# Kernel tuning notes

Hardware: AMD Instinct MI355X
Metric: run time of the kernel (lower is better)

Reference implementation:

```python
import jax, jax.numpy as jnp
import numpy as np

N_SRC = 100000
N_DST = 20000
N_EDGES = 640000
D_IN = 128
D_OUT = 128


def setup_inputs() -> dict:
    key = jax.random.key(0)
    ks = jax.random.split(key, 6)
    feat_src = jax.random.normal(ks[0], (N_SRC, D_IN), dtype=jnp.float32)
    feat_dst = jax.random.normal(ks[1], (N_DST, D_IN), dtype=jnp.float32)
    src_idx = jax.random.randint(ks[2], (N_EDGES,), 0, N_SRC, dtype=jnp.int64 if jax.config.jax_enable_x64 else jnp.int32)
    dst_idx = jax.random.randint(ks[3], (N_EDGES,), 0, N_DST, dtype=jnp.int64 if jax.config.jax_enable_x64 else jnp.int32)
    # xavier-uniform-ish init scale for [out, in] Linear weights
    lim = float(np.sqrt(6.0 / (D_IN + D_OUT)))
    W_self = jax.random.uniform(ks[4], (D_OUT, D_IN), jnp.float32, -lim, lim)
    W_neigh = jax.random.uniform(ks[5], (D_OUT, D_IN), jnp.float32, -lim, lim)
    b_self = jnp.zeros((D_OUT,), jnp.float32)
    b_neigh = jnp.zeros((D_OUT,), jnp.float32)
    return {
        "feat_src": feat_src, "feat_dst": feat_dst,
        "src_idx": src_idx, "dst_idx": dst_idx,
        "W_self": W_self, "b_self": b_self,
        "W_neigh": W_neigh, "b_neigh": b_neigh,
    }


def reference(feat_src, feat_dst, src_idx, dst_idx, W_self, b_self, W_neigh, b_neigh):
    n_dst = feat_dst.shape[0]
    # message passing: copy_src + mean reduce over incoming edges per dst node
    msgs = feat_src[src_idx]                                   # [E, D_in]
    summed = jax.ops.segment_sum(msgs, dst_idx, num_segments=n_dst)  # [N_dst, D_in]
    deg = jax.ops.segment_sum(jnp.ones((src_idx.shape[0],), feat_src.dtype),
                              dst_idx, num_segments=n_dst)     # [N_dst]
    h_neigh = summed / jnp.maximum(deg, 1.0)[:, None]          # mean (0 for isolated)
    # rst = fc_self(h_self) + fc_neigh(h_neigh); no activation
    rst = (feat_dst @ W_self.T + b_self) + (h_neigh @ W_neigh.T + b_neigh)
    return rst
```

## Files before the change

### kernel.cpp

```cpp
#include <hip/hip_runtime.h>

#define D 128
#define NDST 20000
#define NHB 64
#define CAP 96

typedef __attribute__((ext_vector_type(8))) short short8;
typedef __attribute__((ext_vector_type(4))) float f32x4;
typedef __attribute__((ext_vector_type(2))) float f32x2;

__device__ __forceinline__ unsigned f2bf(float f) {
  unsigned x = __float_as_uint(f);
  return (x + 0x7FFFu + ((x >> 16) & 1u)) >> 16;
}
__device__ __forceinline__ unsigned pack2(float a, float b) {
  return f2bf(a) | (f2bf(b) << 16);
}
__device__ __forceinline__ unsigned pack_fp8x4(float a, float b, float c, float d) {
  int v = 0;
  v = __builtin_amdgcn_cvt_pk_fp8_f32(a, b, v, false);
  v = __builtin_amdgcn_cvt_pk_fp8_f32(c, d, v, true);
  return (unsigned)v;
}

__global__ __launch_bounds__(512) void k1(
    const int* __restrict__ dst_idx,
    const float* __restrict__ feat_src,
    const float* __restrict__ feat_dst,
    const float* __restrict__ W_self,
    const float* __restrict__ b_self,
    const float* __restrict__ b_neigh,
    unsigned char* __restrict__ blockHist8,
    unsigned short* __restrict__ rank16,
    unsigned char* __restrict__ fsrc8,
    float* __restrict__ out,
    int n_src, int n_dst, int n_edges, int EPB, int NCB)
{
  __shared__ __align__(16) unsigned char ldsb[43520];
  const int tid = threadIdx.x;
  const int bid = blockIdx.x;

  if (bid < NHB) {
    unsigned int* hist = reinterpret_cast<unsigned int*>(ldsb);
    for (int i = tid; i < NDST / 16; i += 512)
      reinterpret_cast<uint4*>(hist)[i] = make_uint4(0u, 0u, 0u, 0u);
    __syncthreads();
    const int e0 = bid * EPB;
    const int e1 = min(e0 + EPB, n_edges);
    for (int e = e0 + tid; e < e1; e += 512) {
      int d = dst_idx[e];
      int sh = (d & 3) << 3;
      unsigned old = atomicAdd(&hist[d >> 2], 1u << sh);
      rank16[e] = (unsigned short)((old >> sh) & 0xFFu);
    }
    __syncthreads();
    uint4* rowp = reinterpret_cast<uint4*>(blockHist8 + (size_t)bid * NDST);
    const uint4* h4 = reinterpret_cast<const uint4*>(hist);
    for (int i = tid; i < NDST / 16; i += 512) rowp[i] = h4[i];
  } else if (bid < NHB + NCB) {
    const long long NCONV = (long long)n_src * 16;
    const long long NU = NCONV + 16;
    const long long stride = (long long)NCB * 512;
    long long u = (long long)(bid - NHB) * 512 + tid;
    for (; u < NU; u += stride) {
      if (u < NCONV) {
        long long e = u * 8;
        const float4* p = reinterpret_cast<const float4*>(feat_src + e);
        float4 a = p[0], b = p[1];
        uint2 o;
        o.x = pack_fp8x4(a.x, a.y, a.z, a.w);
        o.y = pack_fp8x4(b.x, b.y, b.z, b.w);
        *reinterpret_cast<uint2*>(fsrc8 + e) = o;
      } else {
        *reinterpret_cast<uint2*>(fsrc8 + (size_t)n_src * D + (u - NCONV) * 8) =
            make_uint2(0u, 0u);
      }
    }
  } else {
    unsigned short (*As)[136] = reinterpret_cast<unsigned short (*)[136]>(ldsb);
    unsigned short (*Bs)[136] =
        reinterpret_cast<unsigned short (*)[136]>(ldsb + 32 * 136 * 2);
    const int w = tid >> 6;
    const int lane = tid & 63;
    const int row0 = (bid - NHB - NCB) * 32;

    {
      int r = tid >> 4;
      int q = tid & 15;
      int gr = row0 + r;
      uint4 o = make_uint4(0u, 0u, 0u, 0u);
      if (gr < n_dst) {
        const float4* p = reinterpret_cast<const float4*>(
            feat_dst + (size_t)gr * D + q * 8);
        float4 a = p[0], b = p[1];
        o.x = pack2(a.x, a.y); o.y = pack2(a.z, a.w);
        o.z = pack2(b.x, b.y); o.w = pack2(b.z, b.w);
      }
      *reinterpret_cast<uint4*>(&As[r][q * 8]) = o;
    }
    {
      int n = tid >> 2;
      int q = tid & 3;
      const float4* p = reinterpret_cast<const float4*>(
          W_self + (size_t)n * D + q * 32);
      #pragma unroll
      for (int h = 0; h < 4; ++h) {
        float4 a = p[2 * h], b = p[2 * h + 1];
        uint4 o;
        o.x = pack2(a.x, a.y); o.y = pack2(a.z, a.w);
        o.z = pack2(b.x, b.y); o.w = pack2(b.z, b.w);
        *reinterpret_cast<uint4*>(&Bs[n][q * 32 + h * 8]) = o;
      }
    }
    __syncthreads();

    const int m  = w & 1;
    const int n0 = (w >> 1) * 2;
    const int ar = m * 16 + (lane & 15);
    const int kb = (lane >> 4) * 8;
    f32x4 acc2[2];
    acc2[0] = (f32x4){0.f, 0.f, 0.f, 0.f};
    acc2[1] = (f32x4){0.f, 0.f, 0.f, 0.f};
    #pragma unroll
    for (int kh = 0; kh < 4; ++kh) {
      short8 a = *reinterpret_cast<const short8*>(&As[ar][kh * 32 + kb]);
      #pragma unroll
      for (int t2 = 0; t2 < 2; ++t2) {
        short8 b = *reinterpret_cast<const short8*>(
            &Bs[(n0 + t2) * 16 + (lane & 15)][kh * 32 + kb]);
        acc2[t2] = __builtin_amdgcn_mfma_f32_16x16x32_bf16(a, b, acc2[t2], 0, 0, 0);
      }
    }
    const int r0 = row0 + m * 16 + (lane >> 4) * 4;
    #pragma unroll
    for (int t2 = 0; t2 < 2; ++t2) {
      int col = (n0 + t2) * 16 + (lane & 15);
      float bv = b_self[col] + b_neigh[col];
      #pragma unroll
      for (int r = 0; r < 4; ++r) {
        int gr = r0 + r;
        if (gr < n_dst) out[(size_t)gr * D + col] = acc2[t2][r] + bv;
      }
    }
  }
}

__global__ __launch_bounds__(256) void pB(
    unsigned char* __restrict__ blockHist8,
    int* __restrict__ degi,
    int n_dst)
{
  int d = blockIdx.x * 256 + threadIdx.x;
  if (d >= n_dst) return;
  unsigned char* col = blockHist8 + d;
  unsigned run = 0;
  #pragma unroll 8
  for (int b = 0; b < NHB; ++b) {
    unsigned h = col[(size_t)b * NDST];
    col[(size_t)b * NDST] = (unsigned char)run;
    run += h;
  }
  degi[d] = (int)run;
}

__global__ __launch_bounds__(256) void p3(
    const int* __restrict__ src_idx,
    const int* __restrict__ dst_idx,
    const unsigned short* __restrict__ rank16,
    const unsigned char* __restrict__ blockBase8,
    int* __restrict__ bucket,
    int n_edges, int EPB)
{
  int e0 = (blockIdx.x * 256 + threadIdx.x) * 4;
  if (e0 >= n_edges) return;
  if (e0 + 4 <= n_edges) {
    int4 s4 = *reinterpret_cast<const int4*>(src_idx + e0);
    int4 d4 = *reinterpret_cast<const int4*>(dst_idx + e0);
    ushort4 r4 = *reinterpret_cast<const ushort4*>(rank16 + e0);
    int ds[4] = {d4.x, d4.y, d4.z, d4.w};
    int ss[4] = {s4.x, s4.y, s4.z, s4.w};
    unsigned rr[4] = {r4.x, r4.y, r4.z, r4.w};
    #pragma unroll
    for (int j = 0; j < 4; ++j) {
      int hb = (e0 + j) / EPB;
      unsigned slot = (unsigned)blockBase8[(size_t)hb * NDST + ds[j]] + rr[j];
      if (slot < CAP) bucket[(size_t)ds[j] * CAP + slot] = ss[j];
    }
  } else {
    for (int e = e0; e < n_edges; ++e) {
      int d = dst_idx[e];
      int hb = e / EPB;
      unsigned slot = (unsigned)blockBase8[(size_t)hb * NDST + d] + rank16[e];
      if (slot < CAP) bucket[(size_t)d * CAP + slot] = src_idx[e];
    }
  }
}

__global__ __launch_bounds__(512) void tail(
    const unsigned char* __restrict__ fsrc8,
    const int* __restrict__ degi,
    const int* __restrict__ bucket,
    const float* __restrict__ W_neigh,
    float* __restrict__ out,
    int n_src, int n_dst)
{
  __shared__ unsigned short Ah[32][136];
  __shared__ unsigned short Bs[128][136];

  const int tid  = threadIdx.x;
  const int w    = tid >> 6;
  const int lane = tid & 63;
  const int row0 = blockIdx.x * 32;

  {
    const int g = lane >> 4;
    const int c = lane & 15;
    const uint2* fs2 = reinterpret_cast<const uint2*>(fsrc8);

    for (int it = 0; it < 4; ++it) {
      int row = w * 4 + it;
      int gr = row0 + row;
      if (gr >= n_dst) {
        if (lane < 16)
          *reinterpret_cast<uint4*>(&Ah[row][c * 8]) = make_uint4(0u,0u,0u,0u);
        continue;
      }
      const int total = degi[gr];
      const int use = min(total, CAP);
      const int* brow = bucket + (size_t)gr * CAP;

      float acc[8];
      #pragma unroll
      for (int j = 0; j < 8; ++j) acc[j] = 0.f;

      for (int i = g; i < use; i += 16) {
        int s0 = brow[i];
        int s1 = (i + 4  < use) ? brow[i + 4]  : n_src;
        int s2 = (i + 8  < use) ? brow[i + 8]  : n_src;
        int s3 = (i + 12 < use) ? brow[i + 12] : n_src;
        uint2 v0 = fs2[(size_t)s0 * 16 + c];
        uint2 v1 = fs2[(size_t)s1 * 16 + c];
        uint2 v2 = fs2[(size_t)s2 * 16 + c];
        uint2 v3 = fs2[(size_t)s3 * 16 + c];
        #pragma unroll
        for (int k = 0; k < 4; ++k) {
          unsigned wx = (k == 0) ? v0.x : (k == 1) ? v1.x : (k == 2) ? v2.x : v3.x;
          unsigned wy = (k == 0) ? v0.y : (k == 1) ? v1.y : (k == 2) ? v2.y : v3.y;
          f32x2 a0 = __builtin_amdgcn_cvt_pk_f32_fp8(wx, false);
          f32x2 a1 = __builtin_amdgcn_cvt_pk_f32_fp8(wx, true);
          f32x2 a2 = __builtin_amdgcn_cvt_pk_f32_fp8(wy, false);
          f32x2 a3 = __builtin_amdgcn_cvt_pk_f32_fp8(wy, true);
          acc[0] += a0.x; acc[1] += a0.y; acc[2] += a1.x; acc[3] += a1.y;
          acc[4] += a2.x; acc[5] += a2.y; acc[6] += a3.x; acc[7] += a3.y;
        }
      }

      #pragma unroll
      for (int j = 0; j < 8; ++j) {
        acc[j] += __shfl_xor(acc[j], 16);
        acc[j] += __shfl_xor(acc[j], 32);
      }

      if (lane < 16) {
        float inv = 1.0f / fmaxf((float)total, 1.0f);
        uint4 o;
        o.x = pack2(acc[0] * inv, acc[1] * inv);
        o.y = pack2(acc[2] * inv, acc[3] * inv);
        o.z = pack2(acc[4] * inv, acc[5] * inv);
        o.w = pack2(acc[6] * inv, acc[7] * inv);
        *reinterpret_cast<uint4*>(&Ah[row][c * 8]) = o;
      }
    }
  }
  __syncthreads();

  {
    int n = tid >> 2;
    int q = tid & 3;
    const float4* p = reinterpret_cast<const float4*>(
        W_neigh + (size_t)n * D + q * 32);
    #pragma unroll
    for (int h = 0; h < 4; ++h) {
      float4 a = p[2 * h], b = p[2 * h + 1];
      uint4 o;
      o.x = pack2(a.x, a.y); o.y = pack2(a.z, a.w);
      o.z = pack2(b.x, b.y); o.w = pack2(b.z, b.w);
      *reinterpret_cast<uint4*>(&Bs[n][q * 32 + h * 8]) = o;
    }
  }
  __syncthreads();

  const int m  = w & 1;
  const int n0 = (w >> 1) * 2;
  const int ar = m * 16 + (lane & 15);
  const int kb = (lane >> 4) * 8;

  f32x4 acc2[2];
  acc2[0] = (f32x4){0.f, 0.f, 0.f, 0.f};
  acc2[1] = (f32x4){0.f, 0.f, 0.f, 0.f};

  #pragma unroll
  for (int kh = 0; kh < 4; ++kh) {
    short8 a = *reinterpret_cast<const short8*>(&Ah[ar][kh * 32 + kb]);
    #pragma unroll
    for (int t2 = 0; t2 < 2; ++t2) {
      short8 b = *reinterpret_cast<const short8*>(
          &Bs[(n0 + t2) * 16 + (lane & 15)][kh * 32 + kb]);
      acc2[t2] = __builtin_amdgcn_mfma_f32_16x16x32_bf16(a, b, acc2[t2], 0, 0, 0);
    }
  }

  const int r0 = row0 + m * 16 + (lane >> 4) * 4;
  #pragma unroll
  for (int t2 = 0; t2 < 2; ++t2) {
    int col = (n0 + t2) * 16 + (lane & 15);
    #pragma unroll
    for (int r = 0; r < 4; ++r) {
      int gr = r0 + r;
      if (gr < n_dst) {
        size_t idx = (size_t)gr * D + col;
        out[idx] = out[idx] + acc2[t2][r];
      }
    }
  }
}

extern "C" void kernel_launch(void* const* d_in, const int* in_sizes, int n_in,
                              void* d_out, int out_size, void* d_ws, size_t ws_size,
                              hipStream_t stream) {
  const float* feat_src = (const float*)d_in[0];
  const float* feat_dst = (const float*)d_in[1];
  const int*   src_idx  = (const int*)d_in[2];
  const int*   dst_idx  = (const int*)d_in[3];
  const float* W_self   = (const float*)d_in[4];
  const float* b_self   = (const float*)d_in[5];
  const float* W_neigh  = (const float*)d_in[6];
  const float* b_neigh  = (const float*)d_in[7];
  float* out = (float*)d_out;

  const int n_src   = in_sizes[0] / D;
  const int n_dst   = in_sizes[1] / D;
  const int n_edges = in_sizes[2];

  unsigned char* fsrc8 = (unsigned char*)d_ws;
  int* degi   = (int*)(fsrc8 + (size_t)(n_src + 1) * D);
  int* bucket = degi + NDST;
  unsigned short* rank16 = (unsigned short*)(bucket + (size_t)NDST * CAP);
  unsigned char* blockHist8 = (unsigned char*)(rank16 + n_edges);

  const int EPB = (n_edges + NHB - 1) / NHB;
  const int NCB = 256;
  const int NG  = (n_dst + 31) / 32;

  k1<<<NHB + NCB + NG, 512, 0, stream>>>(
      dst_idx, feat_src, feat_dst, W_self, b_self, b_neigh,
      blockHist8, rank16, fsrc8, out, n_src, n_dst, n_edges, EPB, NCB);

  pB<<<(n_dst + 255) / 256, 256, 0, stream>>>(blockHist8, degi, n_dst);

  p3<<<(n_edges / 4 + 255) / 256, 256, 0, stream>>>(
      src_idx, dst_idx, rank16, blockHist8, bucket, n_edges, EPB);

  tail<<<NG, 512, 0, stream>>>(
      fsrc8, degi, bucket, W_neigh, out, n_src, n_dst);
}
```

Before: 66.17 us.

## Drop prefix-sum kernel; compute bucket bases and degrees inline from fewer histograms

Cuts the number of histogram blocks from 64 to 8 and removes the separate pB prefix-scan kernel. The scatter kernel now sums the preceding per-block histogram entries for each edge, and the tail kernel rebuilds the degree with a wave shuffle reduction over the 8 histogram rows. Edge ranks shrink from 16-bit to 8-bit. This saves one launch and a pass over the histograms, but each of the 8 histogram blocks now processes 80k edges with LDS atomics, so the critical path in k1 gets longer. Per-block 8-bit counts can also overflow more easily.

```diff
diff --git a/kernel.cpp b/kernel.cpp
--- a/kernel.cpp
+++ b/kernel.cpp
@@ -2,7 +2,7 @@
 
 #define D 128
 #define NDST 20000
-#define NHB 64
+#define NHB 8
 #define CAP 96
 
 typedef __attribute__((ext_vector_type(8))) short short8;
@@ -30,8 +30,8 @@
     const float* __restrict__ W_self,
     const float* __restrict__ b_self,
     const float* __restrict__ b_neigh,
-    unsigned char* __restrict__ blockHist8,
-    unsigned short* __restrict__ rank16,
+    unsigned char* __restrict__ hist8,
+    unsigned char* __restrict__ rank8,
     unsigned char* __restrict__ fsrc8,
     float* __restrict__ out,
     int n_src, int n_dst, int n_edges, int EPB, int NCB)
@@ -51,10 +51,10 @@
       int d = dst_idx[e];
       int sh = (d & 3) << 3;
       unsigned old = atomicAdd(&hist[d >> 2], 1u << sh);
-      rank16[e] = (unsigned short)((old >> sh) & 0xFFu);
+      rank8[e] = (unsigned char)((old >> sh) & 0xFFu);
     }
     __syncthreads();
-    uint4* rowp = reinterpret_cast<uint4*>(blockHist8 + (size_t)bid * NDST);
+    uint4* rowp = reinterpret_cast<uint4*>(hist8 + (size_t)bid * NDST);
     const uint4* h4 = reinterpret_cast<const uint4*>(hist);
     for (int i = tid; i < NDST / 16; i += 512) rowp[i] = h4[i];
   } else if (bid < NHB + NCB) {
@@ -145,29 +145,11 @@
   }
 }
 
-__global__ __launch_bounds__(256) void pB(
-    unsigned char* __restrict__ blockHist8,
-    int* __restrict__ degi,
-    int n_dst)
-{
-  int d = blockIdx.x * 256 + threadIdx.x;
-  if (d >= n_dst) return;
-  unsigned char* col = blockHist8 + d;
-  unsigned run = 0;
-  #pragma unroll 8
-  for (int b = 0; b < NHB; ++b) {
-    unsigned h = col[(size_t)b * NDST];
-    col[(size_t)b * NDST] = (unsigned char)run;
-    run += h;
-  }
-  degi[d] = (int)run;
-}
-
 __global__ __launch_bounds__(256) void p3(
     const int* __restrict__ src_idx,
     const int* __restrict__ dst_idx,
-    const unsigned short* __restrict__ rank16,
-    const unsigned char* __restrict__ blockBase8,
+    const unsigned char* __restrict__ rank8,
+    const unsigned char* __restrict__ hist8,
     int* __restrict__ bucket,
     int n_edges, int EPB)
 {
@@ -176,21 +158,25 @@
   if (e0 + 4 <= n_edges) {
     int4 s4 = *reinterpret_cast<const int4*>(src_idx + e0);
     int4 d4 = *reinterpret_cast<const int4*>(dst_idx + e0);
-    ushort4 r4 = *reinterpret_cast<const ushort4*>(rank16 + e0);
+    uchar4 r4 = *reinterpret_cast<const uchar4*>(rank8 + e0);
     int ds[4] = {d4.x, d4.y, d4.z, d4.w};
     int ss[4] = {s4.x, s4.y, s4.z, s4.w};
     unsigned rr[4] = {r4.x, r4.y, r4.z, r4.w};
     #pragma unroll
     for (int j = 0; j < 4; ++j) {
       int hb = (e0 + j) / EPB;
-      unsigned slot = (unsigned)blockBase8[(size_t)hb * NDST + ds[j]] + rr[j];
+      unsigned base = 0;
+      for (int b = 0; b < hb; ++b) base += hist8[(size_t)b * NDST + ds[j]];
+      unsigned slot = base + rr[j];
       if (slot < CAP) bucket[(size_t)ds[j] * CAP + slot] = ss[j];
     }
   } else {
     for (int e = e0; e < n_edges; ++e) {
       int d = dst_idx[e];
       int hb = e / EPB;
-      unsigned slot = (unsigned)blockBase8[(size_t)hb * NDST + d] + rank16[e];
+      unsigned base = 0;
+      for (int b = 0; b < hb; ++b) base += hist8[(size_t)b * NDST + d];
+      unsigned slot = base + rank8[e];
       if (slot < CAP) bucket[(size_t)d * CAP + slot] = src_idx[e];
     }
   }
@@ -198,7 +184,7 @@
 
 __global__ __launch_bounds__(512) void tail(
     const unsigned char* __restrict__ fsrc8,
-    const int* __restrict__ degi,
+    const unsigned char* __restrict__ hist8,
     const int* __restrict__ bucket,
     const float* __restrict__ W_neigh,
     float* __restrict__ out,
@@ -225,7 +211,11 @@
           *reinterpret_cast<uint4*>(&Ah[row][c * 8]) = make_uint4(0u,0u,0u,0u);
         continue;
       }
-      const int total = degi[gr];
+      unsigned dv = (lane < NHB) ? (unsigned)hist8[(size_t)lane * NDST + gr] : 0u;
+      dv += __shfl_xor(dv, 1);
+      dv += __shfl_xor(dv, 2);
+      dv += __shfl_xor(dv, 4);
+      const int total = (int)__shfl(dv, 0);
       const int use = min(total, CAP);
       const int* brow = bucket + (size_t)gr * CAP;
 
@@ -343,10 +333,9 @@
   const int n_edges = in_sizes[2];
 
   unsigned char* fsrc8 = (unsigned char*)d_ws;
-  int* degi   = (int*)(fsrc8 + (size_t)(n_src + 1) * D);
-  int* bucket = degi + NDST;
-  unsigned short* rank16 = (unsigned short*)(bucket + (size_t)NDST * CAP);
-  unsigned char* blockHist8 = (unsigned char*)(rank16 + n_edges);
+  int* bucket = (int*)(fsrc8 + (size_t)(n_src + 1) * D);
+  unsigned char* rank8 = (unsigned char*)(bucket + (size_t)NDST * CAP);
+  unsigned char* hist8 = rank8 + (((size_t)n_edges + 15) & ~(size_t)15);
 
   const int EPB = (n_edges + NHB - 1) / NHB;
   const int NCB = 256;
@@ -354,13 +343,11 @@
 
   k1<<<NHB + NCB + NG, 512, 0, stream>>>(
       dst_idx, feat_src, feat_dst, W_self, b_self, b_neigh,
-      blockHist8, rank16, fsrc8, out, n_src, n_dst, n_edges, EPB, NCB);
-
-  pB<<<(n_dst + 255) / 256, 256, 0, stream>>>(blockHist8, degi, n_dst);
+      hist8, rank8, fsrc8, out, n_src, n_dst, n_edges, EPB, NCB);
 
   p3<<<(n_edges / 4 + 255) / 256, 256, 0, stream>>>(
-      src_idx, dst_idx, rank16, blockHist8, bucket, n_edges, EPB);
+      src_idx, dst_idx, rank8, hist8, bucket, n_edges, EPB);
 
   tail<<<NG, 512, 0, stream>>>(
-      fsrc8, degi, bucket, W_neigh, out, n_src, n_dst);
-}
+      fsrc8, hist8, bucket, W_neigh, out, n_src, n_dst);
+}
```

Measured after the change: 101.5 us. 53.5% more time.
